# Kernel optimization log

Hardware: AMD Instinct MI355X
Metric: run time of the kernel (lower is better)

Reference implementation:

```python
import jax, jax.numpy as jnp
import numpy as np

B, C, H, W = 4, 64, 64, 64
C2 = 2 * C
CR = C2 // 16  # SE bottleneck

def setup_inputs() -> dict:
    key = jax.random.key(0)
    ks = jax.random.split(key, 8)
    stdv = 1.0 / np.sqrt(C)
    return {
        "x1": jax.random.normal(ks[0], (B, C, H, W), jnp.float32),
        "x2": jax.random.normal(ks[1], (B, C, H, W), jnp.float32),
        "weight": jax.random.uniform(ks[2], (C, C), jnp.float32, -stdv, stdv),
        "weight2": jax.random.uniform(ks[3], (C, C), jnp.float32, -stdv, stdv),
        "ca_fc1": jax.random.normal(ks[4], (CR, C2), jnp.float32) * 0.05,  # 1x1 conv as matrix
        "ca_fc2": jax.random.normal(ks[5], (C2, CR), jnp.float32) * 0.05,
        "conv_w": jax.random.normal(ks[6], (C, C2), jnp.float32) * 0.05,  # 1x1 conv 2C->C
        "conv_b": jnp.zeros((C,), jnp.float32),
    }

def reference(x1, x2, weight, weight2, ca_fc1, ca_fc2, conv_w, conv_b):
    b, c, h, w = x2.shape
    n = h * w
    a1 = x1.reshape(b, c, n)  # x1 flattened [B,C,N]
    a2 = x2.reshape(b, c, n)  # x2 flattened [B,C,N]
    # Non-local branch: f = theta_x @ phi_x = a1^T @ a2 -> [B,N,N]
    f = jnp.einsum('bcn,bcm->bnm', a1, a2)
    adj = jax.nn.softmax(f, axis=-1)
    support = jnp.einsum('bcn,cd->bnd', a2, weight)  # g_x @ W, [B,N,C]
    y = jnp.einsum('bnm,bmd->bnd', adj, support)     # adj @ support
    y = y.transpose(0, 2, 1).reshape(b, c, h, w)
    # Channel-affinity branch: c_x = a_x @ b_x -> [B,C,C]
    c_x = jnp.einsum('bcn,bdn->bcd', a1, a2)
    support2 = jnp.einsum('bcd,de->bce', c_x, weight2)   # [B,C,C]
    y2 = jnp.einsum('bcd,bdn->bcn', support2, a1).reshape(b, c, h, w)
    z = jnp.concatenate([y, y2], axis=1)  # [B,2C,H,W]
    # ChannelAttention: global max pool -> fc1 -> relu -> fc2 -> sigmoid
    mp = jnp.max(z, axis=(2, 3))                       # [B,2C]
    hdn = jax.nn.relu(jnp.einsum('be,re->br', mp, ca_fc1))
    v = jax.nn.sigmoid(jnp.einsum('br,er->be', hdn, ca_fc2))  # [B,2C]
    out = z * v[:, :, None, None] + z
    out = jnp.einsum('behw,oe->bohw', out, conv_w) + conv_b[None, :, None, None]
    return out
```

## Files before the change

### kernel.cpp

```cpp
#include <hip/hip_runtime.h>
#include <hip/hip_bf16.h>
#include <math.h>

#define B_   4
#define C_   64
#define N_   4096
#define C2_  128

using frag  = __attribute__((ext_vector_type(8))) short;
using f32x4 = __attribute__((ext_vector_type(4))) float;
using f4    = __attribute__((ext_vector_type(4))) float;

__device__ __forceinline__ unsigned short f2bf(float f) {
  unsigned int u = __float_as_uint(f);
  u += 0x7fffu + ((u >> 16) & 1u);
  return (unsigned short)(u >> 16);
}
__device__ __forceinline__ float bf2f(unsigned short h) {
  return __uint_as_float(((unsigned int)h) << 16);
}
__device__ __forceinline__ unsigned int pkbf(float a, float b) {
  __hip_bfloat16 ha = __float2bfloat16(a), hb = __float2bfloat16(b);
  unsigned short ua, ub;
  __builtin_memcpy(&ua, &ha, 2);
  __builtin_memcpy(&ub, &hb, 2);
  return (unsigned int)ua | ((unsigned int)ub << 16);
}
__device__ __forceinline__ frag pk8(f4 lo, f4 hi) {
  frag f;
  unsigned int* u = (unsigned int*)&f;
  u[0] = pkbf(lo.x, lo.y);
  u[1] = pkbf(lo.z, lo.w);
  u[2] = pkbf(hi.x, hi.y);
  u[3] = pkbf(hi.z, hi.w);
  return f;
}
__device__ __forceinline__ f4 max4(f4 a, f4 b) {
  return (f4){fmaxf(a.x, b.x), fmaxf(a.y, b.y), fmaxf(a.z, b.z), fmaxf(a.w, b.w)};
}

__global__ __launch_bounds__(256) void prep_kernel(const float* __restrict__ x1,
                                                   const float* __restrict__ x2,
                                                   unsigned short* __restrict__ a1t,
                                                   unsigned short* __restrict__ a2t,
                                                   float* __restrict__ cxp) {
  __shared__ float tA[64 * 65];
  __shared__ float tB[64 * 65];
  int b = blockIdx.y, n0 = blockIdx.x * 64, tid = threadIdx.x;
  int wave = tid >> 6, lane = tid & 63, l16 = lane & 15, lq = lane >> 4;
  {
    int n = tid & 63, cq = tid >> 6;
#pragma unroll
    for (int k = 0; k < 16; ++k) {
      int c = cq + 4 * k;
      tA[c * 65 + n] = x2[((size_t)(b * C_ + c)) * N_ + n0 + n];
      tB[c * 65 + n] = x1[((size_t)(b * C_ + c)) * N_ + n0 + n];
    }
  }
  __syncthreads();
  {
    int c = tid & 63, nq = tid >> 6;
#pragma unroll
    for (int k = 0; k < 16; ++k) {
      int n2 = nq + 4 * k;
      a2t[((size_t)b * N_ + n0 + n2) * C_ + c] = f2bf(tA[c * 65 + n2]);
      a1t[((size_t)b * N_ + n0 + n2) * C_ + c] = f2bf(tB[c * 65 + n2]);
    }
  }
  {
    int dd = 16 * wave + l16;
    frag afr[2];
#pragma unroll
    for (int ks = 0; ks < 2; ++ks) {
      float w0[8];
#pragma unroll
      for (int j = 0; j < 8; ++j) w0[j] = tA[dd * 65 + ks * 32 + lq * 8 + j];
      afr[ks] = pk8((f4){w0[0], w0[1], w0[2], w0[3]}, (f4){w0[4], w0[5], w0[6], w0[7]});
    }
    f32x4 acc[4];
#pragma unroll
    for (int cg = 0; cg < 4; ++cg) acc[cg] = (f32x4){0.f, 0.f, 0.f, 0.f};
#pragma unroll
    for (int cg = 0; cg < 4; ++cg) {
      int cc = cg * 16 + l16;
#pragma unroll
      for (int ks = 0; ks < 2; ++ks) {
        float w0[8];
#pragma unroll
        for (int j = 0; j < 8; ++j) w0[j] = tB[cc * 65 + ks * 32 + lq * 8 + j];
        frag bfr = pk8((f4){w0[0], w0[1], w0[2], w0[3]}, (f4){w0[4], w0[5], w0[6], w0[7]});
        acc[cg] = __builtin_amdgcn_mfma_f32_16x16x32_bf16(afr[ks], bfr, acc[cg], 0, 0, 0);
      }
    }
    float* op = cxp + ((size_t)(b * 64 + blockIdx.x)) * 4096;
#pragma unroll
    for (int cg = 0; cg < 4; ++cg)
#pragma unroll
      for (int r = 0; r < 4; ++r)
        op[(16 * wave + 4 * lq + r) * 64 + cg * 16 + l16] = acc[cg][r];
  }
}

__global__ __launch_bounds__(256) void support_mm_kernel(const float* __restrict__ weight,
                                                         const unsigned short* __restrict__ a2t,
                                                         unsigned short* __restrict__ vT) {
  __shared__ float Wl[64 * 65];
  int b = blockIdx.y, n0 = blockIdx.x * 32, tid = threadIdx.x;
  int wave = tid >> 6, lane = tid & 63, l16 = lane & 15, lq = lane >> 4;
#pragma unroll
  for (int k = 0; k < 16; ++k) {
    int lin = tid + 256 * k;
    Wl[(lin >> 6) * 65 + (lin & 63)] = weight[lin];
  }
  frag b0[2], b1[2];
#pragma unroll
  for (int ng = 0; ng < 2; ++ng) {
    const unsigned short* bp = a2t + ((size_t)b * N_ + n0 + ng * 16 + l16) * C_;
    b0[ng] = *(const frag*)(bp + lq * 8);
    b1[ng] = *(const frag*)(bp + 32 + lq * 8);
  }
  __syncthreads();
  int dd = 16 * wave + l16;
  frag aw[2];
#pragma unroll
  for (int ks = 0; ks < 2; ++ks) {
    float wv[8];
#pragma unroll
    for (int j = 0; j < 8; ++j) wv[j] = Wl[(ks * 32 + lq * 8 + j) * 65 + dd];
    aw[ks] = pk8((f4){wv[0], wv[1], wv[2], wv[3]}, (f4){wv[4], wv[5], wv[6], wv[7]});
  }
  f32x4 acc[2];
#pragma unroll
  for (int ng = 0; ng < 2; ++ng) {
    acc[ng] = (f32x4){0.f, 0.f, 0.f, 0.f};
    acc[ng] = __builtin_amdgcn_mfma_f32_16x16x32_bf16(aw[0], b0[ng], acc[ng], 0, 0, 0);
    acc[ng] = __builtin_amdgcn_mfma_f32_16x16x32_bf16(aw[1], b1[ng], acc[ng], 0, 0, 0);
  }
#pragma unroll
  for (int ng = 0; ng < 2; ++ng)
#pragma unroll
    for (int r = 0; r < 4; ++r)
      vT[((size_t)(b * C_) + 16 * wave + 4 * lq + r) * N_ + n0 + ng * 16 + l16] =
          f2bf(acc[ng][r]);
}

__global__ __launch_bounds__(256) void cxred_kernel(const float* __restrict__ cxp,
                                                    float* __restrict__ cx) {
  int idx = blockIdx.x * 256 + threadIdx.x;
  int b = idx >> 12, r = idx & 4095;
  const float* p = cxp + (size_t)b * 64 * 4096 + r;
  float s = 0.f;
#pragma unroll 8
  for (int sg = 0; sg < 64; ++sg) s += p[(size_t)sg * 4096];
  cx[idx] = s;
}

__global__ __launch_bounds__(256) void s2bf_kernel(const float* __restrict__ cx,
                                                   const float* __restrict__ w2,
                                                   unsigned short* __restrict__ s2bf) {
  __shared__ float cxl[4096];
  __shared__ float w2l[4096];
  int b = blockIdx.x, tid = threadIdx.x;
#pragma unroll
  for (int k = 0; k < 16; ++k) {
    int lin = tid + 256 * k;
    cxl[lin] = cx[(size_t)b * 4096 + lin];
    w2l[lin] = w2[lin];
  }
  __syncthreads();
  int c = tid & 63, eg = tid >> 6;
  float acc[16];
#pragma unroll
  for (int i = 0; i < 16; ++i) acc[i] = 0.f;
  for (int d = 0; d < 64; ++d) {
    float a = cxl[d * 64 + c];
#pragma unroll
    for (int i = 0; i < 16; ++i) acc[i] += a * w2l[d * 64 + eg * 16 + i];
  }
  unsigned short* op = s2bf + (size_t)b * 4096 + c * 64 + eg * 16;
#pragma unroll
  for (int i = 0; i < 8; ++i)
    *(unsigned int*)(op + 2 * i) = pkbf(acc[2 * i], acc[2 * i + 1]);
}

template <int SEG>
__global__ __launch_bounds__(512) void attn_kernel(const unsigned short* __restrict__ a1t,
                                                   const unsigned short* __restrict__ a2t,
                                                   const unsigned short* __restrict__ vT,
                                                   float* __restrict__ z,
                                                   unsigned short* __restrict__ Opart,
                                                   float* __restrict__ ml) {
  __shared__ unsigned short Kt[2][64 * 64];
  __shared__ unsigned short Vt[2][64 * 64];
  __shared__ uint2 Pl[8][16 * 16];

  const int b = blockIdx.y, n0 = blockIdx.x * 128, tid = threadIdx.x;
  const int seg = (SEG > 1) ? blockIdx.z : 0;
  const int wave = tid >> 6, lane = tid & 63;
  const int l16 = lane & 15, lq = lane >> 4;
  const int NT = N_ / SEG / 64;
  const int mbase = seg * (N_ / SEG);

  const unsigned short* qbase = a1t + ((size_t)b * N_ + n0 + wave * 16 + l16) * C_;
  frag qa0 = *(const frag*)(qbase + lq * 8);
  frag qa1 = *(const frag*)(qbase + 32 + lq * 8);

  f32x4 O[4];
#pragma unroll
  for (int i = 0; i < 4; ++i) O[i] = (f32x4){0.f, 0.f, 0.f, 0.f};
  float m_l = -1e30f, l_l = 0.f;

  const unsigned short* a2b = a2t + (size_t)b * N_ * C_;
  const unsigned short* vTb = vT + (size_t)b * C_ * N_;
  char* Pw = (char*)&Pl[wave][0];
  const int swzP = (l16 & 7) << 4;

  const int srow = tid >> 3, scb = tid & 7;
  const int kswz = (scb * 16) ^ ((srow & 7) << 4);

  frag k0 = *(const frag*)(a2b + (size_t)(mbase + srow) * C_ + scb * 8);
  frag v0 = *(const frag*)(vTb + (size_t)srow * N_ + mbase + scb * 8);
  *(frag*)((char*)&Kt[0][0] + srow * 128 + kswz) = k0;
  *(frag*)((char*)&Vt[0][0] + srow * 128 + kswz) = v0;
  __syncthreads();

  int cur = 0;
  for (int t = 0; t < NT; ++t, cur ^= 1) {
    if (t + 1 < NT) {
      int mn = mbase + (t + 1) * 64;
      k0 = *(const frag*)(a2b + (size_t)(mn + srow) * C_ + scb * 8);
      v0 = *(const frag*)(vTb + (size_t)srow * N_ + mn + scb * 8);
    }

    f32x4 S[4];
    __builtin_amdgcn_s_setprio(1);
#pragma unroll
    for (int ms = 0; ms < 4; ++ms) {
      int m = ms * 16 + l16;
      int swz = (m & 7) << 4;
      frag kb0 = *(const frag*)((char*)&Kt[cur][0] + m * 128 + ((lq * 16) ^ swz));
      frag kb1 = *(const frag*)((char*)&Kt[cur][0] + m * 128 + ((64 + lq * 16) ^ swz));
      f32x4 acc = (f32x4){0.f, 0.f, 0.f, 0.f};
      acc = __builtin_amdgcn_mfma_f32_16x16x32_bf16(kb0, qa0, acc, 0, 0, 0);
      acc = __builtin_amdgcn_mfma_f32_16x16x32_bf16(kb1, qa1, acc, 0, 0, 0);
      S[ms] = acc;
    }
    __builtin_amdgcn_s_setprio(0);

    float mx0 = fmaxf(fmaxf(S[0][0], S[0][1]), fmaxf(S[0][2], S[0][3]));
    float mx1 = fmaxf(fmaxf(S[1][0], S[1][1]), fmaxf(S[1][2], S[1][3]));
    float mx2 = fmaxf(fmaxf(S[2][0], S[2][1]), fmaxf(S[2][2], S[2][3]));
    float mx3 = fmaxf(fmaxf(S[3][0], S[3][1]), fmaxf(S[3][2], S[3][3]));
    float mx = fmaxf(fmaxf(mx0, mx1), fmaxf(mx2, mx3));
    mx = fmaxf(mx, __shfl_xor(mx, 16, 64));
    mx = fmaxf(mx, __shfl_xor(mx, 32, 64));

    if (!__all(mx <= m_l + 8.f)) {
      float mn = fmaxf(m_l, mx);
      float sc = __expf(m_l - mn);
      m_l = mn;
      l_l *= sc;
      float scb_[4];
#pragma unroll
      for (int r = 0; r < 4; ++r) scb_[r] = __shfl(sc, 20 * lq + r, 64);
#pragma unroll
      for (int ds = 0; ds < 4; ++ds)
#pragma unroll
        for (int r = 0; r < 4; ++r) O[ds][r] *= scb_[r];
    }

    float p[16];
    float rs = 0.f;
#pragma unroll
    for (int ms = 0; ms < 4; ++ms)
#pragma unroll
      for (int r = 0; r < 4; ++r) {
        float e = __expf(S[ms][r] - m_l);
        p[ms * 4 + r] = e;
        rs += e;
      }
    rs += __shfl_xor(rs, 16, 64);
    rs += __shfl_xor(rs, 32, 64);
    l_l += rs;

#pragma unroll
    for (int ms = 0; ms < 4; ++ms) {
      uint2 w;
      w.x = pkbf(p[ms * 4 + 0], p[ms * 4 + 1]);
      w.y = pkbf(p[ms * 4 + 2], p[ms * 4 + 3]);
      *(uint2*)(Pw + l16 * 128 + ((32 * ms + 8 * lq) ^ swzP)) = w;
    }
    asm volatile("s_waitcnt lgkmcnt(0)" ::: "memory");
    __builtin_amdgcn_sched_barrier(0);

    frag pa0 = *(const frag*)(Pw + l16 * 128 + ((lq * 16) ^ swzP));
    frag pa1 = *(const frag*)(Pw + l16 * 128 + ((64 + lq * 16) ^ swzP));
    __builtin_amdgcn_s_setprio(1);
#pragma unroll
    for (int ds = 0; ds < 4; ++ds) {
      int d = ds * 16 + l16;
      int swz = (d & 7) << 4;
      frag vb0 = *(const frag*)((char*)&Vt[cur][0] + d * 128 + ((lq * 16) ^ swz));
      frag vb1 = *(const frag*)((char*)&Vt[cur][0] + d * 128 + ((64 + lq * 16) ^ swz));
      O[ds] = __builtin_amdgcn_mfma_f32_16x16x32_bf16(pa0, vb0, O[ds], 0, 0, 0);
      O[ds] = __builtin_amdgcn_mfma_f32_16x16x32_bf16(pa1, vb1, O[ds], 0, 0, 0);
    }
    __builtin_amdgcn_s_setprio(0);

    if (t + 1 < NT) {
      *(frag*)((char*)&Kt[cur ^ 1][0] + srow * 128 + kswz) = k0;
      *(frag*)((char*)&Vt[cur ^ 1][0] + srow * 128 + kswz) = v0;
      __syncthreads();
    }
  }

  if (SEG > 1) {
    size_t base = (size_t)(b * SEG + seg) * N_ + n0 + wave * 16;
    if (lq == 0) {
      ml[(base + l16) * 2]     = m_l;
      ml[(base + l16) * 2 + 1] = l_l;
    }
#pragma unroll
    for (int r = 0; r < 4; ++r)
#pragma unroll
      for (int ds = 0; ds < 4; ++ds)
        Opart[(base + lq * 4 + r) * 64 + ds * 16 + l16] = f2bf(O[ds][r]);
  } else {
    float inv[4];
#pragma unroll
    for (int r = 0; r < 4; ++r) inv[r] = 1.f / __shfl(l_l, 20 * lq + r, 64);
#pragma unroll
    for (int ds = 0; ds < 4; ++ds)
#pragma unroll
      for (int r = 0; r < 4; ++r)
        z[((size_t)b * N_ + n0 + wave * 16 + lq * 4 + r) * 128 + ds * 16 + l16] = O[ds][r] * inv[r];
  }
}

__global__ __launch_bounds__(256) void combine_kernel(const unsigned short* __restrict__ Opart,
                                                      const float* __restrict__ ml,
                                                      float* __restrict__ z,
                                                      float* __restrict__ mppA) {
  __shared__ float zsm[64][65];
  int b = blockIdx.y, tid = threadIdx.x;
  int nr = tid >> 2;
  int n = blockIdx.x * 64 + nr;
  int dq = (tid & 3) * 16;
  float mv[4], lv[4], M = -1e30f;
#pragma unroll
  for (int s = 0; s < 4; ++s) {
    size_t r = (size_t)(b * 4 + s) * N_ + n;
    mv[s] = ml[r * 2];
    lv[s] = ml[r * 2 + 1];
    M = fmaxf(M, mv[s]);
  }
  float acc[16];
#pragma unroll
  for (int j = 0; j < 16; ++j) acc[j] = 0.f;
  float l = 0.f;
#pragma unroll
  for (int s = 0; s < 4; ++s) {
    float w = __expf(mv[s] - M);
    l += w * lv[s];
    const unsigned short* op = Opart + ((size_t)(b * 4 + s) * N_ + n) * 64 + dq;
    frag p0 = *(const frag*)(op);
    frag p1 = *(const frag*)(op + 8);
#pragma unroll
    for (int j = 0; j < 8; ++j) {
      acc[j]     += w * bf2f((unsigned short)p0[j]);
      acc[8 + j] += w * bf2f((unsigned short)p1[j]);
    }
  }
  float inv = 1.f / l;
  float* zp = z + ((size_t)b * N_ + n) * 128 + dq;
#pragma unroll
  for (int k = 0; k < 4; ++k) {
    f4 res = (f4){acc[4 * k] * inv, acc[4 * k + 1] * inv,
                  acc[4 * k + 2] * inv, acc[4 * k + 3] * inv};
    *(f4*)(zp + k * 4) = res;
    zsm[nr][dq + 4 * k]     = res.x;
    zsm[nr][dq + 4 * k + 1] = res.y;
    zsm[nr][dq + 4 * k + 2] = res.z;
    zsm[nr][dq + 4 * k + 3] = res.w;
  }
  __syncthreads();
  if (tid < 64) {
    float mx = -1e30f;
    for (int nn = 0; nn < 64; ++nn) mx = fmaxf(mx, zsm[nn][tid]);
    mppA[((size_t)b * 64 + blockIdx.x) * 64 + tid] = mx;
  }
}

__global__ __launch_bounds__(256) void mpA_kernel(const float* __restrict__ z,
                                                  float* __restrict__ mppA) {
  __shared__ float red[4][64];
  int b = blockIdx.y, n0 = blockIdx.x * 64, tid = threadIdx.x;
  int e = tid & 63, g = tid >> 6;
  float mx = -1e30f;
#pragma unroll
  for (int k = 0; k < 16; ++k)
    mx = fmaxf(mx, z[((size_t)b * N_ + n0 + g + 4 * k) * 128 + e]);
  red[g][e] = mx;
  __syncthreads();
  if (tid < 64)
    mppA[((size_t)b * 64 + blockIdx.x) * 64 + tid] =
        fmaxf(fmaxf(red[0][tid], red[1][tid]), fmaxf(red[2][tid], red[3][tid]));
}

__global__ __launch_bounds__(256) void y2_kernel(const unsigned short* __restrict__ s2bf,
                                                 const unsigned short* __restrict__ a1t,
                                                 float* __restrict__ z,
                                                 float* __restrict__ mppB) {
  __shared__ f4 red[4][4][16];
  int b = blockIdx.y, n0 = blockIdx.x * 32, tid = threadIdx.x;
  int wave = tid >> 6, lane = tid & 63, l16 = lane & 15, lq = lane >> 4;
  const unsigned short* s2r = s2bf + (size_t)b * 4096 + (16 * wave + l16) * 64;
  frag sa0 = *(const frag*)(s2r + lq * 8);
  frag sa1 = *(const frag*)(s2r + 32 + lq * 8);
  f4 mx = (f4){-1e30f, -1e30f, -1e30f, -1e30f};
#pragma unroll
  for (int j = 0; j < 2; ++j) {
    const unsigned short* bp = a1t + ((size_t)b * N_ + n0 + 16 * j + l16) * 64;
    frag b0 = *(const frag*)(bp + lq * 8);
    frag b1 = *(const frag*)(bp + 32 + lq * 8);
    f32x4 acc = (f32x4){0.f, 0.f, 0.f, 0.f};
    acc = __builtin_amdgcn_mfma_f32_16x16x32_bf16(sa0, b0, acc, 0, 0, 0);
    acc = __builtin_amdgcn_mfma_f32_16x16x32_bf16(sa1, b1, acc, 0, 0, 0);
    *(f4*)(z + ((size_t)b * N_ + n0 + 16 * j + l16) * 128 + 64 + 16 * wave + 4 * lq) = acc;
#pragma unroll
    for (int r = 0; r < 4; ++r) mx[r] = fmaxf(mx[r], acc[r]);
  }
  red[wave][lq][l16] = mx;
  __syncthreads();
  if (tid < 64) {
    int w = tid >> 4, q = (tid >> 2) & 3, r = tid & 3;
    float m = -1e30f;
#pragma unroll
    for (int l = 0; l < 16; ++l) m = fmaxf(m, red[w][q][l][r]);
    mppB[((size_t)b * 128 + blockIdx.x) * 64 + 16 * w + 4 * q + r] = m;
  }
}

__global__ __launch_bounds__(256) void ca2_kernel(const float* __restrict__ mppA,
                                                  const float* __restrict__ mppB,
                                                  const float* __restrict__ fc1,
                                                  const float* __restrict__ fc2,
                                                  float* __restrict__ vbuf) {
  __shared__ f4 red4[256];
  __shared__ float mpl[128];
  __shared__ float red2[8][33];
  __shared__ float hl[8];
  int b = blockIdx.x, t = threadIdx.x;
  {
    const f4* src = (const f4*)(mppA + (size_t)b * 64 * 64);
    f4 m = src[t];
    m = max4(m, src[t + 256]);
    m = max4(m, src[t + 512]);
    m = max4(m, src[t + 768]);
    red4[t] = m;
  }
  __syncthreads();
  if (t < 16) {
    f4 m = red4[t];
#pragma unroll
    for (int j = 1; j < 16; ++j) m = max4(m, red4[t + 16 * j]);
    *(f4*)&mpl[t * 4] = m;
  }
  __syncthreads();
  {
    const f4* src = (const f4*)(mppB + (size_t)b * 128 * 64);
    f4 m = src[t];
#pragma unroll
    for (int k = 1; k < 8; ++k) m = max4(m, src[t + 256 * k]);
    red4[t] = m;
  }
  __syncthreads();
  if (t < 16) {
    f4 m = red4[t];
#pragma unroll
    for (int j = 1; j < 16; ++j) m = max4(m, red4[t + 16 * j]);
    *(f4*)&mpl[64 + t * 4] = m;
  }
  __syncthreads();
  {
    int r = t >> 5, j = t & 31;
    const f4 mv = *(const f4*)&mpl[j * 4];
    const f4 wv = *(const f4*)(fc1 + r * 128 + j * 4);
    red2[r][j] = mv.x * wv.x + mv.y * wv.y + mv.z * wv.z + mv.w * wv.w;
  }
  __syncthreads();
  if (t < 8) {
    float s = 0.f;
#pragma unroll
    for (int j = 0; j < 32; ++j) s += red2[t][j];
    hl[t] = fmaxf(s, 0.f);
  }
  __syncthreads();
  if (t < 128) {
    float s = 0.f;
    const float* f2r = fc2 + t * 8;
#pragma unroll
    for (int r = 0; r < 8; ++r) s += hl[r] * f2r[r];
    vbuf[b * 128 + t] = 1.f + 1.f / (1.f + __expf(-s));
  }
}

__global__ __launch_bounds__(256) void conv_kernel(const float* __restrict__ z,
                                                   const float* __restrict__ vbuf,
                                                   const float* __restrict__ conv_w,
                                                   const float* __restrict__ conv_b,
                                                   float* __restrict__ out) {
  __shared__ unsigned short zv[64 * 128];
  int b = blockIdx.y, n0 = blockIdx.x * 64, tid = threadIdx.x;
  int wave = tid >> 6, lane = tid & 63, l16 = lane & 15, lq = lane >> 4;
  {
    int e4 = tid & 31;
    f4 vq = *(const f4*)(vbuf + b * 128 + e4 * 4);
#pragma unroll
    for (int k = 0; k < 8; ++k) {
      int row = (tid >> 5) + 8 * k;
      f4 zq = *(const f4*)(z + ((size_t)(b * N_) + n0 + row) * 128 + e4 * 4);
      zq *= vq;
      uint2 w;
      w.x = pkbf(zq.x, zq.y);
      w.y = pkbf(zq.z, zq.w);
      *(uint2*)((char*)zv + row * 256 + ((e4 * 8) ^ ((row & 7) << 4))) = w;
    }
  }
  const float* cwr = conv_w + (size_t)(16 * wave + l16) * 128 + lq * 8;
  frag aw[4];
#pragma unroll
  for (int ks = 0; ks < 4; ++ks)
    aw[ks] = pk8(*(const f4*)(cwr + ks * 32), *(const f4*)(cwr + ks * 32 + 4));
  __syncthreads();
  f32x4 acc[4];
#pragma unroll
  for (int ng = 0; ng < 4; ++ng) acc[ng] = (f32x4){0.f, 0.f, 0.f, 0.f};
#pragma unroll
  for (int ng = 0; ng < 4; ++ng) {
    int n = ng * 16 + l16;
    int swz = (n & 7) << 4;
#pragma unroll
    for (int ks = 0; ks < 4; ++ks) {
      frag bz = *(const frag*)((char*)zv + n * 256 + ((ks * 64 + lq * 16) ^ swz));
      acc[ng] = __builtin_amdgcn_mfma_f32_16x16x32_bf16(aw[ks], bz, acc[ng], 0, 0, 0);
    }
  }
#pragma unroll
  for (int r = 0; r < 4; ++r) {
    int o = 16 * wave + 4 * lq + r;
    float bias = conv_b[o];
#pragma unroll
    for (int ng = 0; ng < 4; ++ng)
      out[((size_t)(b * C_ + o)) * N_ + n0 + ng * 16 + l16] = acc[ng][r] + bias;
  }
}

extern "C" void kernel_launch(void* const* d_in, const int* in_sizes, int n_in,
                              void* d_out, int out_size, void* d_ws, size_t ws_size,
                              hipStream_t stream) {
  const float* x1      = (const float*)d_in[0];
  const float* x2      = (const float*)d_in[1];
  const float* weight  = (const float*)d_in[2];
  const float* weight2 = (const float*)d_in[3];
  const float* fc1     = (const float*)d_in[4];
  const float* fc2     = (const float*)d_in[5];
  const float* conv_w  = (const float*)d_in[6];
  const float* conv_b  = (const float*)d_in[7];
  float* out = (float*)d_out;

  char* ws = (char*)d_ws;
  unsigned short* a1t = (unsigned short*)(ws + 0);
  unsigned short* a2t = (unsigned short*)(ws + 2097152);
  float* mppA = (float*)(ws + 2097152);
  float* mppB = (float*)(ws + 2162688);
  unsigned short* s2bf = (unsigned short*)(ws + 2293760);
  unsigned short* vT  = (unsigned short*)(ws + 4194304);
  float* z    = (float*)(ws + 6291456);
  float* cxp  = (float*)(ws + 6291456);
  float* cx   = (float*)(ws + 14680064);
  float* vbuf = (float*)(ws + 14745600);
  unsigned short* Opart = (unsigned short*)(ws + 14764544);
  float* ml   = (float*)(ws + 23153152);
  const bool seg4 = ws_size >= 23677440ull;

  prep_kernel<<<dim3(64, 4), 256, 0, stream>>>(x1, x2, a1t, a2t, cxp);
  support_mm_kernel<<<dim3(128, 4), 256, 0, stream>>>(weight, a2t, vT);
  cxred_kernel<<<dim3(64), 256, 0, stream>>>(cxp, cx);
  if (seg4) {
    attn_kernel<4><<<dim3(32, 4, 4), 512, 0, stream>>>(a1t, a2t, vT, z, Opart, ml);
    combine_kernel<<<dim3(64, 4), 256, 0, stream>>>(Opart, ml, z, mppA);
  } else {
    attn_kernel<1><<<dim3(32, 4), 512, 0, stream>>>(a1t, a2t, vT, z, nullptr, nullptr);
    mpA_kernel<<<dim3(64, 4), 256, 0, stream>>>(z, mppA);
  }
  s2bf_kernel<<<dim3(4), 256, 0, stream>>>(cx, weight2, s2bf);
  y2_kernel<<<dim3(128, 4), 256, 0, stream>>>(s2bf, a1t, z, mppB);
  ca2_kernel<<<dim3(4), 256, 0, stream>>>(mppA, mppB, fc1, fc2, vbuf);
  conv_kernel<<<dim3(64, 4), 256, 0, stream>>>(z, vbuf, conv_w, conv_b, out);
}
```

Measured before the change: 74.59 us.

## Split attention into eight KV segments, fuse y2 into combine, shrink prep tiles

Adds an eight-segment split-KV attention path, used when the workspace is large enough, to raise the number of blocks launched. It fuses the y2 channel-affinity matmul and its max reduction into the softmax combine kernel, which drops one launch and lets y2 reuse the combine blocks, each now covering 64 positions. The prep kernel moves to 32-position tiles with twice as many blocks, and the cx partial reduction now sums 128 partials. The tradeoffs are more partial-output traffic and combine work, and the eight-segment path depends on workspace size.

After: 78.70 us. +5.5%, slower.

```diff
diff --git a/kernel.cpp b/kernel.cpp
--- a/kernel.cpp
+++ b/kernel.cpp
@@ -44,55 +44,46 @@
                                                    unsigned short* __restrict__ a1t,
                                                    unsigned short* __restrict__ a2t,
                                                    float* __restrict__ cxp) {
-  __shared__ float tA[64 * 65];
-  __shared__ float tB[64 * 65];
-  int b = blockIdx.y, n0 = blockIdx.x * 64, tid = threadIdx.x;
+  __shared__ float tA[64 * 33];
+  __shared__ float tB[64 * 33];
+  int b = blockIdx.y, n0 = blockIdx.x * 32, tid = threadIdx.x;
   int wave = tid >> 6, lane = tid & 63, l16 = lane & 15, lq = lane >> 4;
   {
-    int n = tid & 63, cq = tid >> 6;
-#pragma unroll
-    for (int k = 0; k < 16; ++k) {
-      int c = cq + 4 * k;
-      tA[c * 65 + n] = x2[((size_t)(b * C_ + c)) * N_ + n0 + n];
-      tB[c * 65 + n] = x1[((size_t)(b * C_ + c)) * N_ + n0 + n];
+    int n = tid & 31, cq = tid >> 5;
+#pragma unroll
+    for (int k = 0; k < 8; ++k) {
+      int c = cq + 8 * k;
+      tA[c * 33 + n] = x2[((size_t)(b * C_ + c)) * N_ + n0 + n];
+      tB[c * 33 + n] = x1[((size_t)(b * C_ + c)) * N_ + n0 + n];
     }
   }
   __syncthreads();
   {
     int c = tid & 63, nq = tid >> 6;
 #pragma unroll
-    for (int k = 0; k < 16; ++k) {
+    for (int k = 0; k < 8; ++k) {
       int n2 = nq + 4 * k;
-      a2t[((size_t)b * N_ + n0 + n2) * C_ + c] = f2bf(tA[c * 65 + n2]);
-      a1t[((size_t)b * N_ + n0 + n2) * C_ + c] = f2bf(tB[c * 65 + n2]);
+      a2t[((size_t)b * N_ + n0 + n2) * C_ + c] = f2bf(tA[c * 33 + n2]);
+      a1t[((size_t)b * N_ + n0 + n2) * C_ + c] = f2bf(tB[c * 33 + n2]);
     }
   }
   {
     int dd = 16 * wave + l16;
-    frag afr[2];
-#pragma unroll
-    for (int ks = 0; ks < 2; ++ks) {
-      float w0[8];
-#pragma unroll
-      for (int j = 0; j < 8; ++j) w0[j] = tA[dd * 65 + ks * 32 + lq * 8 + j];
-      afr[ks] = pk8((f4){w0[0], w0[1], w0[2], w0[3]}, (f4){w0[4], w0[5], w0[6], w0[7]});
-    }
+    float w0[8];
+#pragma unroll
+    for (int j = 0; j < 8; ++j) w0[j] = tA[dd * 33 + lq * 8 + j];
+    frag afr = pk8((f4){w0[0], w0[1], w0[2], w0[3]}, (f4){w0[4], w0[5], w0[6], w0[7]});
     f32x4 acc[4];
-#pragma unroll
-    for (int cg = 0; cg < 4; ++cg) acc[cg] = (f32x4){0.f, 0.f, 0.f, 0.f};
 #pragma unroll
     for (int cg = 0; cg < 4; ++cg) {
       int cc = cg * 16 + l16;
 #pragma unroll
-      for (int ks = 0; ks < 2; ++ks) {
-        float w0[8];
-#pragma unroll
-        for (int j = 0; j < 8; ++j) w0[j] = tB[cc * 65 + ks * 32 + lq * 8 + j];
-        frag bfr = pk8((f4){w0[0], w0[1], w0[2], w0[3]}, (f4){w0[4], w0[5], w0[6], w0[7]});
-        acc[cg] = __builtin_amdgcn_mfma_f32_16x16x32_bf16(afr[ks], bfr, acc[cg], 0, 0, 0);
-      }
-    }
-    float* op = cxp + ((size_t)(b * 64 + blockIdx.x)) * 4096;
+      for (int j = 0; j < 8; ++j) w0[j] = tB[cc * 33 + lq * 8 + j];
+      frag bfr = pk8((f4){w0[0], w0[1], w0[2], w0[3]}, (f4){w0[4], w0[5], w0[6], w0[7]});
+      acc[cg] = (f32x4){0.f, 0.f, 0.f, 0.f};
+      acc[cg] = __builtin_amdgcn_mfma_f32_16x16x32_bf16(afr, bfr, acc[cg], 0, 0, 0);
+    }
+    float* op = cxp + ((size_t)(b * 128 + blockIdx.x)) * 4096;
 #pragma unroll
     for (int cg = 0; cg < 4; ++cg)
 #pragma unroll
@@ -148,10 +139,10 @@
                                                     float* __restrict__ cx) {
   int idx = blockIdx.x * 256 + threadIdx.x;
   int b = idx >> 12, r = idx & 4095;
-  const float* p = cxp + (size_t)b * 64 * 4096 + r;
+  const float* p = cxp + (size_t)b * 128 * 4096 + r;
   float s = 0.f;
 #pragma unroll 8
-  for (int sg = 0; sg < 64; ++sg) s += p[(size_t)sg * 4096];
+  for (int sg = 0; sg < 128; ++sg) s += p[(size_t)sg * 4096];
   cx[idx] = s;
 }
 
@@ -337,19 +328,59 @@
   }
 }
 
-__global__ __launch_bounds__(256) void combine_kernel(const unsigned short* __restrict__ Opart,
-                                                      const float* __restrict__ ml,
-                                                      float* __restrict__ z,
-                                                      float* __restrict__ mppA) {
+__device__ __forceinline__ void y2_phase(const unsigned short* __restrict__ s2bf,
+                                         const unsigned short* __restrict__ a1t,
+                                         float* __restrict__ z,
+                                         float* __restrict__ mppB,
+                                         f4 (*red)[4][16],
+                                         int b, int blkx, int tid) {
+  int n0 = blkx * 64;
+  int wave = tid >> 6, lane = tid & 63, l16 = lane & 15, lq = lane >> 4;
+  const unsigned short* s2r = s2bf + (size_t)b * 4096 + (16 * wave + l16) * 64;
+  frag sa0 = *(const frag*)(s2r + lq * 8);
+  frag sa1 = *(const frag*)(s2r + 32 + lq * 8);
+  f4 mx = (f4){-1e30f, -1e30f, -1e30f, -1e30f};
+#pragma unroll
+  for (int ng = 0; ng < 4; ++ng) {
+    const unsigned short* bp = a1t + ((size_t)b * N_ + n0 + ng * 16 + l16) * 64;
+    frag b0 = *(const frag*)(bp + lq * 8);
+    frag b1 = *(const frag*)(bp + 32 + lq * 8);
+    f32x4 acc = (f32x4){0.f, 0.f, 0.f, 0.f};
+    acc = __builtin_amdgcn_mfma_f32_16x16x32_bf16(sa0, b0, acc, 0, 0, 0);
+    acc = __builtin_amdgcn_mfma_f32_16x16x32_bf16(sa1, b1, acc, 0, 0, 0);
+    *(f4*)(z + ((size_t)b * N_ + n0 + ng * 16 + l16) * 128 + 64 + 16 * wave + 4 * lq) = acc;
+#pragma unroll
+    for (int r = 0; r < 4; ++r) mx[r] = fmaxf(mx[r], acc[r]);
+  }
+  red[wave][lq][l16] = mx;
+  __syncthreads();
+  if (tid < 64) {
+    int w = tid >> 4, q = (tid >> 2) & 3, r = tid & 3;
+    float m = -1e30f;
+#pragma unroll
+    for (int l = 0; l < 16; ++l) m = fmaxf(m, red[w][q][l][r]);
+    mppB[((size_t)b * 64 + blkx) * 64 + 16 * w + 4 * q + r] = m;
+  }
+}
+
+template <int SEG>
+__global__ __launch_bounds__(256) void combineY2_kernel(const unsigned short* __restrict__ Opart,
+                                                        const float* __restrict__ ml,
+                                                        const unsigned short* __restrict__ s2bf,
+                                                        const unsigned short* __restrict__ a1t,
+                                                        float* __restrict__ z,
+                                                        float* __restrict__ mppA,
+                                                        float* __restrict__ mppB) {
   __shared__ float zsm[64][65];
+  __shared__ f4 red[4][4][16];
   int b = blockIdx.y, tid = threadIdx.x;
   int nr = tid >> 2;
   int n = blockIdx.x * 64 + nr;
   int dq = (tid & 3) * 16;
-  float mv[4], lv[4], M = -1e30f;
-#pragma unroll
-  for (int s = 0; s < 4; ++s) {
-    size_t r = (size_t)(b * 4 + s) * N_ + n;
+  float mv[SEG], lv[SEG], M = -1e30f;
+#pragma unroll
+  for (int s = 0; s < SEG; ++s) {
+    size_t r = (size_t)(b * SEG + s) * N_ + n;
     mv[s] = ml[r * 2];
     lv[s] = ml[r * 2 + 1];
     M = fmaxf(M, mv[s]);
@@ -359,10 +390,10 @@
   for (int j = 0; j < 16; ++j) acc[j] = 0.f;
   float l = 0.f;
 #pragma unroll
-  for (int s = 0; s < 4; ++s) {
+  for (int s = 0; s < SEG; ++s) {
     float w = __expf(mv[s] - M);
     l += w * lv[s];
-    const unsigned short* op = Opart + ((size_t)(b * 4 + s) * N_ + n) * 64 + dq;
+    const unsigned short* op = Opart + ((size_t)(b * SEG + s) * N_ + n) * 64 + dq;
     frag p0 = *(const frag*)(op);
     frag p1 = *(const frag*)(op + 8);
 #pragma unroll
@@ -389,6 +420,7 @@
     for (int nn = 0; nn < 64; ++nn) mx = fmaxf(mx, zsm[nn][tid]);
     mppA[((size_t)b * 64 + blockIdx.x) * 64 + tid] = mx;
   }
+  y2_phase(s2bf, a1t, z, mppB, red, b, blockIdx.x, tid);
 }
 
 __global__ __launch_bounds__(256) void mpA_kernel(const float* __restrict__ z,
@@ -412,33 +444,7 @@
                                                  float* __restrict__ z,
                                                  float* __restrict__ mppB) {
   __shared__ f4 red[4][4][16];
-  int b = blockIdx.y, n0 = blockIdx.x * 32, tid = threadIdx.x;
-  int wave = tid >> 6, lane = tid & 63, l16 = lane & 15, lq = lane >> 4;
-  const unsigned short* s2r = s2bf + (size_t)b * 4096 + (16 * wave + l16) * 64;
-  frag sa0 = *(const frag*)(s2r + lq * 8);
-  frag sa1 = *(const frag*)(s2r + 32 + lq * 8);
-  f4 mx = (f4){-1e30f, -1e30f, -1e30f, -1e30f};
-#pragma unroll
-  for (int j = 0; j < 2; ++j) {
-    const unsigned short* bp = a1t + ((size_t)b * N_ + n0 + 16 * j + l16) * 64;
-    frag b0 = *(const frag*)(bp + lq * 8);
-    frag b1 = *(const frag*)(bp + 32 + lq * 8);
-    f32x4 acc = (f32x4){0.f, 0.f, 0.f, 0.f};
-    acc = __builtin_amdgcn_mfma_f32_16x16x32_bf16(sa0, b0, acc, 0, 0, 0);
-    acc = __builtin_amdgcn_mfma_f32_16x16x32_bf16(sa1, b1, acc, 0, 0, 0);
-    *(f4*)(z + ((size_t)b * N_ + n0 + 16 * j + l16) * 128 + 64 + 16 * wave + 4 * lq) = acc;
-#pragma unroll
-    for (int r = 0; r < 4; ++r) mx[r] = fmaxf(mx[r], acc[r]);
-  }
-  red[wave][lq][l16] = mx;
-  __syncthreads();
-  if (tid < 64) {
-    int w = tid >> 4, q = (tid >> 2) & 3, r = tid & 3;
-    float m = -1e30f;
-#pragma unroll
-    for (int l = 0; l < 16; ++l) m = fmaxf(m, red[w][q][l][r]);
-    mppB[((size_t)b * 128 + blockIdx.x) * 64 + 16 * w + 4 * q + r] = m;
-  }
+  y2_phase(s2bf, a1t, z, mppB, red, blockIdx.y, blockIdx.x, threadIdx.x);
 }
 
 __global__ __launch_bounds__(256) void ca2_kernel(const float* __restrict__ mppA,
@@ -468,10 +474,11 @@
   }
   __syncthreads();
   {
-    const f4* src = (const f4*)(mppB + (size_t)b * 128 * 64);
+    const f4* src = (const f4*)(mppB + (size_t)b * 64 * 64);
     f4 m = src[t];
-#pragma unroll
-    for (int k = 1; k < 8; ++k) m = max4(m, src[t + 256 * k]);
+    m = max4(m, src[t + 256]);
+    m = max4(m, src[t + 512]);
+    m = max4(m, src[t + 768]);
     red4[t] = m;
   }
   __syncthreads();
@@ -581,21 +588,28 @@
   float* cx   = (float*)(ws + 14680064);
   float* vbuf = (float*)(ws + 14745600);
   unsigned short* Opart = (unsigned short*)(ws + 14764544);
-  float* ml   = (float*)(ws + 23153152);
+  float* ml4  = (float*)(ws + 23153152);
+  float* ml8  = (float*)(ws + 31541760);
+  const bool seg8 = ws_size >= 32590336ull;
   const bool seg4 = ws_size >= 23677440ull;
 
-  prep_kernel<<<dim3(64, 4), 256, 0, stream>>>(x1, x2, a1t, a2t, cxp);
+  prep_kernel<<<dim3(128, 4), 256, 0, stream>>>(x1, x2, a1t, a2t, cxp);
   support_mm_kernel<<<dim3(128, 4), 256, 0, stream>>>(weight, a2t, vT);
   cxred_kernel<<<dim3(64), 256, 0, stream>>>(cxp, cx);
-  if (seg4) {
-    attn_kernel<4><<<dim3(32, 4, 4), 512, 0, stream>>>(a1t, a2t, vT, z, Opart, ml);
-    combine_kernel<<<dim3(64, 4), 256, 0, stream>>>(Opart, ml, z, mppA);
+  if (seg8) {
+    attn_kernel<8><<<dim3(32, 4, 8), 512, 0, stream>>>(a1t, a2t, vT, z, Opart, ml8);
+    s2bf_kernel<<<dim3(4), 256, 0, stream>>>(cx, weight2, s2bf);
+    combineY2_kernel<8><<<dim3(64, 4), 256, 0, stream>>>(Opart, ml8, s2bf, a1t, z, mppA, mppB);
+  } else if (seg4) {
+    attn_kernel<4><<<dim3(32, 4, 4), 512, 0, stream>>>(a1t, a2t, vT, z, Opart, ml4);
+    s2bf_kernel<<<dim3(4), 256, 0, stream>>>(cx, weight2, s2bf);
+    combineY2_kernel<4><<<dim3(64, 4), 256, 0, stream>>>(Opart, ml4, s2bf, a1t, z, mppA, mppB);
   } else {
     attn_kernel<1><<<dim3(32, 4), 512, 0, stream>>>(a1t, a2t, vT, z, nullptr, nullptr);
+    s2bf_kernel<<<dim3(4), 256, 0, stream>>>(cx, weight2, s2bf);
     mpA_kernel<<<dim3(64, 4), 256, 0, stream>>>(z, mppA);
-  }
-  s2bf_kernel<<<dim3(4), 256, 0, stream>>>(cx, weight2, s2bf);
-  y2_kernel<<<dim3(128, 4), 256, 0, stream>>>(s2bf, a1t, z, mppB);
+    y2_kernel<<<dim3(64, 4), 256, 0, stream>>>(s2bf, a1t, z, mppB);
+  }
   ca2_kernel<<<dim3(4), 256, 0, stream>>>(mppA, mppB, fc1, fc2, vbuf);
   conv_kernel<<<dim3(64, 4), 256, 0, stream>>>(z, vbuf, conv_w, conv_b, out);
 }
```
